# Performance work log

Measured on AMD Instinct MI355X. Metric: run time of the kernel, lower is better.

The kernel has to match this reference:

```python
import jax, jax.numpy as jnp
import numpy as np

H_DIM = 1024
HEAD_SIZE = 1024


def setup_inputs() -> dict:
    key = jax.random.key(0)
    ks = jax.random.split(key, 7)
    s = 1.0 / np.sqrt(H_DIM)
    x = jax.random.normal(ks[0], (4, 4096, H_DIM), dtype=jnp.float32)
    Wq = jax.random.uniform(ks[1], (H_DIM, HEAD_SIZE), jnp.float32, -s, s)
    bq = jax.random.uniform(ks[2], (HEAD_SIZE,), jnp.float32, -s, s)
    Wk = jax.random.uniform(ks[3], (H_DIM, HEAD_SIZE), jnp.float32, -s, s)
    bk = jax.random.uniform(ks[4], (HEAD_SIZE,), jnp.float32, -s, s)
    Wv = jax.random.uniform(ks[5], (H_DIM, HEAD_SIZE), jnp.float32, -s, s)
    bv = jax.random.uniform(ks[6], (HEAD_SIZE,), jnp.float32, -s, s)
    return {"x": x, "Wq": Wq, "bq": bq, "Wk": Wk, "bk": bk, "Wv": Wv, "bv": bv}


def reference(x, Wq, bq, Wk, bk, Wv, bv):
    B, S, _ = x.shape
    q = x @ Wq + bq  # [B,S,hs]
    k = x @ Wk + bk
    v = x @ Wv + bv
    scores = jnp.einsum('bqd,bkd->bqk', q, k)  # [B,S,S]
    causal = jnp.tril(jnp.ones((S, S), dtype=bool))
    scores = jnp.where(causal, scores, -jnp.inf)
    # original divides after masking; -inf stays -inf so math is identical
    w = jax.nn.softmax(scores / jnp.sqrt(jnp.float32(HEAD_SIZE)), axis=-1)
    # dropout p=0.0 -> identity
    return jnp.einsum('bqk,bkd->bqd', w, v)
```

## Files before the change

kernel.cpp:

```cpp
#include <hip/hip_runtime.h>
#include <stdint.h>

typedef _Float16 f16;
typedef _Float16 v8h __attribute__((ext_vector_type(8)));
typedef _Float16 v4h __attribute__((ext_vector_type(4)));
typedef float v4f __attribute__((ext_vector_type(4)));

#define LOG2E 1.44269504088896340736f
#define PT 16384

__device__ __forceinline__ void gll16(const void* g, void* l) {
  __builtin_amdgcn_global_load_lds((__attribute__((address_space(1))) void*)g,
                                   (__attribute__((address_space(3))) void*)l,
                                   16, 0, 0);
}

__device__ __forceinline__ int xcd_swz(int p, int chunk) {
  return (p & 7) * chunk + (p >> 3);
}

__global__ void k_cvt_x(const float* __restrict__ x, f16* __restrict__ xh, int n4) {
  int i = blockIdx.x * blockDim.x + threadIdx.x;
  if (i >= n4) return;
  float4 v = ((const float4*)x)[i];
  v4h o;
  o[0] = (f16)v.x; o[1] = (f16)v.y; o[2] = (f16)v.z; o[3] = (f16)v.w;
  ((v4h*)xh)[i] = o;
}

__global__ void k_cvt_wt(const float* __restrict__ Wq, const float* __restrict__ Wk,
                         const float* __restrict__ Wv, f16* __restrict__ Wt) {
  __shared__ f16 tile[64][65];
  int z = blockIdx.z;
  const float* W = (z == 0) ? Wq : (z == 1) ? Wk : Wv;
  int k0 = blockIdx.y * 64, n0 = blockIdx.x * 64;
  int t = threadIdx.x;
  int r = t >> 4, c4 = t & 15;
  for (int i = 0; i < 4; ++i) {
    int row = r + i * 16;
    float4 v = *(const float4*)&W[(size_t)(k0 + row) * 1024 + n0 + c4 * 4];
    tile[c4 * 4 + 0][row] = (f16)v.x;
    tile[c4 * 4 + 1][row] = (f16)v.y;
    tile[c4 * 4 + 2][row] = (f16)v.z;
    tile[c4 * 4 + 3][row] = (f16)v.w;
  }
  __syncthreads();
  f16* out = Wt + (size_t)z * 1048576;
  for (int i = 0; i < 4; ++i) {
    int n = r + i * 16;
    v4h o;
    o[0] = tile[n][c4 * 4 + 0];
    o[1] = tile[n][c4 * 4 + 1];
    o[2] = tile[n][c4 * 4 + 2];
    o[3] = tile[n][c4 * 4 + 3];
    *(v4h*)&out[(size_t)(n0 + n) * 1024 + k0 + c4 * 4] = o;
  }
}

__global__ __launch_bounds__(512) void k_qkv(
    const f16* __restrict__ xh,
    const f16* __restrict__ Wt,
    const float* __restrict__ bq, const float* __restrict__ bk, const float* __restrict__ bv,
    f16* __restrict__ q, f16* __restrict__ k, f16* __restrict__ vT) {
  __shared__ __align__(16) f16 As[2][16384];
  __shared__ __align__(16) f16 Bs[2][16384];
  int p = blockIdx.x + 64 * (blockIdx.y + 4 * blockIdx.z);
  int l = xcd_swz(p, 96);
  int mt = l / 12;
  int rem = l - mt * 12;
  int z = rem >> 2, nt = rem & 3;
  int m0 = mt * 256, n0 = nt * 256;
  const f16* gA = xh + (size_t)m0 * 1024;
  const f16* gB = Wt + (size_t)z * 1048576 + (size_t)n0 * 1024;
  const float* bias = (z == 0) ? bq : (z == 1) ? bk : bv;
  int tid = threadIdx.x;
  int lane = tid & 63, wave = tid >> 6;
  int quad = lane >> 4, l15 = lane & 15;
  int wm = (wave >> 2) * 128, wn = (wave & 3) * 64;

  int soff[4], slds[4];
#pragma unroll
  for (int h = 0; h < 4; ++h) {
    int s = h * 512 + tid;
    int row = s >> 3;
    int c = (s & 7) ^ (row & 7);
    soff[h] = row * 1024 + c * 8;
    slds[h] = (h * 512 + wave * 64) * 8;
  }
  v4f acc[8][4] = {};
  v8h a[8], bfr[4];

#define QSTAGE(dst, g, kf) do {                                            \
    _Pragma("unroll") for (int h = 0; h < 4; ++h)                          \
      gll16((g) + soff[h] + (kf), &(dst)[slds[h]]);                        \
  } while (0)

#define QREAD(d, ks) do {                                                  \
    int sl = (((ks) * 4 + quad) ^ (l15 & 7)) * 8;                          \
    _Pragma("unroll") for (int i = 0; i < 8; ++i)                          \
      a[i] = *(const v8h*)&As[d][(wm + i * 16 + l15) * 64 + sl];           \
    _Pragma("unroll") for (int j = 0; j < 4; ++j)                          \
      bfr[j] = *(const v8h*)&Bs[d][(wn + j * 16 + l15) * 64 + sl];         \
  } while (0)

#define QMFMA() do {                                                       \
    __builtin_amdgcn_s_setprio(1);                                         \
    _Pragma("unroll") for (int i = 0; i < 8; ++i)                          \
      _Pragma("unroll") for (int j = 0; j < 4; ++j)                        \
        acc[i][j] = __builtin_amdgcn_mfma_f32_16x16x32_f16(a[i], bfr[j], acc[i][j], 0, 0, 0); \
    __builtin_amdgcn_s_setprio(0);                                         \
  } while (0)

  QSTAGE(As[0], gA, 0);
  QSTAGE(Bs[0], gB, 0);

#pragma unroll 1
  for (int it = 0; it < 7; ++it) {
    int k1 = (2 * it + 1) * 64, k2 = (2 * it + 2) * 64;
    QSTAGE(As[1], gA, k1);
    asm volatile("s_waitcnt vmcnt(4)" ::: "memory");
    __builtin_amdgcn_s_barrier();
    QREAD(0, 0); QMFMA();
    QREAD(0, 1);
    QSTAGE(Bs[1], gB, k1);
    QMFMA();
    __builtin_amdgcn_s_barrier();
    QSTAGE(As[0], gA, k2);
    asm volatile("s_waitcnt vmcnt(4)" ::: "memory");
    __builtin_amdgcn_s_barrier();
    QREAD(1, 0); QMFMA();
    QREAD(1, 1);
    QSTAGE(Bs[0], gB, k2);
    QMFMA();
    __builtin_amdgcn_s_barrier();
  }
  {
    int k1 = 15 * 64;
    QSTAGE(As[1], gA, k1);
    asm volatile("s_waitcnt vmcnt(4)" ::: "memory");
    __builtin_amdgcn_s_barrier();
    QREAD(0, 0); QMFMA();
    QREAD(0, 1);
    QSTAGE(Bs[1], gB, k1);
    QMFMA();
    __builtin_amdgcn_s_barrier();
    asm volatile("s_waitcnt vmcnt(0)" ::: "memory");
    __builtin_amdgcn_s_barrier();
    QREAD(1, 0); QMFMA();
    QREAD(1, 1); QMFMA();
  }
#undef QSTAGE
#undef QREAD
#undef QMFMA

  if (z < 2) {
    f16* outp = (z == 0) ? q : k;
    float scale = (z == 0) ? 0.03125f : 1.0f;
#pragma unroll
    for (int j = 0; j < 4; ++j) {
      int n = n0 + wn + j * 16 + l15;
      float bia = bias[n];
#pragma unroll
      for (int i = 0; i < 8; ++i) {
        int mb = m0 + wm + i * 16 + quad * 4;
#pragma unroll
        for (int r = 0; r < 4; ++r)
          outp[(size_t)(mb + r) * 1024 + n] = (f16)((acc[i][j][r] + bia) * scale);
      }
    }
  } else {
#pragma unroll
    for (int j = 0; j < 4; ++j) {
      int n = n0 + wn + j * 16 + l15;
      float bia = bias[n];
#pragma unroll
      for (int i = 0; i < 8; ++i) {
        int m = m0 + wm + i * 16 + quad * 4;
        int bb = m >> 12, s = m & 4095;
        v4h o;
#pragma unroll
        for (int r = 0; r < 4; ++r) o[r] = (f16)(acc[i][j][r] + bia);
        *(v4h*)&vT[((size_t)bb * 1024 + n) * 4096 + s] = o;
      }
    }
  }
}

__global__ void k_zero(float* __restrict__ p) {
  p[blockIdx.x * 256 + threadIdx.x] = 0.f;
}

__global__ __launch_bounds__(256) void k_sgemm(
    const f16* __restrict__ q, const f16* __restrict__ kmat,
    f16* __restrict__ P, float* __restrict__ rowsum, int b0) {
  __shared__ __align__(16) f16 As[2][8192];
  __shared__ __align__(16) f16 Bs[2][8192];
  int p = blockIdx.x + 528 * blockIdx.y;
  int l = xcd_swz(p, 132);
  int i = (l >= 528) ? l - 528 : l;
  int bb = (l >= 528) ? 1 : 0;
  int b = b0 * 2 + bb;
  int mt = (int)((sqrtf(8.f * i + 1.f) - 1.f) * 0.5f);
  while ((mt + 1) * (mt + 2) / 2 <= i) ++mt;
  while (mt * (mt + 1) / 2 > i) --mt;
  int nt = i - mt * (mt + 1) / 2;
  const f16* A = q + ((size_t)b * 4096 + (size_t)mt * 128) * 1024;
  const f16* B = kmat + ((size_t)b * 4096 + (size_t)nt * 128) * 1024;
  f16* Pt = P + (size_t)bb * 528 * PT + (size_t)i * PT;

  int tid = threadIdx.x;
  int lane = tid & 63, wave = tid >> 6;
  int quad = lane >> 4, l15 = lane & 15;
  int wm = (wave & 1) * 64, wn = (wave >> 1) * 64;

  int soff[4], slds[4];
#pragma unroll
  for (int h = 0; h < 4; ++h) {
    int s = h * 256 + tid;
    int row = s >> 3;
    int c = (s & 7) ^ (row & 7);
    soff[h] = row * 1024 + c * 8;
    slds[h] = (h * 256 + wave * 64) * 8;
  }
  v4f acc[4][4] = {};
  v8h a[4], bf[4];

#define SSTAGE(dst, g, kf) do {                                            \
    _Pragma("unroll") for (int h = 0; h < 4; ++h)                          \
      gll16((g) + soff[h] + (kf), &(dst)[slds[h]]);                        \
  } while (0)

#define SREAD(d, ks) do {                                                  \
    int sl = (((ks) * 4 + quad) ^ (l15 & 7)) * 8;                          \
    _Pragma("unroll") for (int ii = 0; ii < 4; ++ii)                       \
      a[ii] = *(const v8h*)&As[d][(wm + ii * 16 + l15) * 64 + sl];         \
    _Pragma("unroll") for (int j = 0; j < 4; ++j)                          \
      bf[j] = *(const v8h*)&Bs[d][(wn + j * 16 + l15) * 64 + sl];          \
  } while (0)

#define SMFMA() do {                                                       \
    __builtin_amdgcn_s_setprio(1);                                         \
    _Pragma("unroll") for (int ii = 0; ii < 4; ++ii)                       \
      _Pragma("unroll") for (int j = 0; j < 4; ++j)                        \
        acc[ii][j] = __builtin_amdgcn_mfma_f32_16x16x32_f16(a[ii], bf[j], acc[ii][j], 0, 0, 0); \
    __builtin_amdgcn_s_setprio(0);                                         \
  } while (0)

  SSTAGE(As[0], A, 0);
  SSTAGE(Bs[0], B, 0);

#pragma unroll 1
  for (int it = 0; it < 7; ++it) {
    int k1 = (2 * it + 1) * 64, k2 = (2 * it + 2) * 64;
    SSTAGE(As[1], A, k1);
    asm volatile("s_waitcnt vmcnt(4)" ::: "memory");
    __builtin_amdgcn_s_barrier();
    SREAD(0, 0); SMFMA();
    SREAD(0, 1);
    SSTAGE(Bs[1], B, k1);
    SMFMA();
    __builtin_amdgcn_s_barrier();
    SSTAGE(As[0], A, k2);
    asm volatile("s_waitcnt vmcnt(4)" ::: "memory");
    __builtin_amdgcn_s_barrier();
    SREAD(1, 0); SMFMA();
    SREAD(1, 1);
    SSTAGE(Bs[0], B, k2);
    SMFMA();
    __builtin_amdgcn_s_barrier();
  }
  {
    int k1 = 15 * 64;
    SSTAGE(As[1], A, k1);
    asm volatile("s_waitcnt vmcnt(4)" ::: "memory");
    __builtin_amdgcn_s_barrier();
    SREAD(0, 0); SMFMA();
    SREAD(0, 1);
    SSTAGE(Bs[1], B, k1);
    SMFMA();
    __builtin_amdgcn_s_barrier();
    asm volatile("s_waitcnt vmcnt(0)" ::: "memory");
    __builtin_amdgcn_s_barrier();
    SREAD(1, 0); SMFMA();
    SREAD(1, 1); SMFMA();
  }
#undef SSTAGE
#undef SREAD
#undef SMFMA

  bool diag = (nt == mt);
  float* rsb = rowsum + (size_t)b * 4096 + mt * 128;
  for (int ii = 0; ii < 4; ++ii) {
    int rl = wm + ii * 16 + quad * 4;
    for (int r = 0; r < 4; ++r) {
      int row_l = rl + r;
      float rs = 0.f;
      for (int j = 0; j < 4; ++j) {
        int col_l = wn + j * 16 + l15;
        float pv = __builtin_amdgcn_exp2f(acc[ii][j][r] * LOG2E);
        if (diag && col_l > row_l) pv = 0.f;
        Pt[(size_t)row_l * 128 + col_l] = (f16)pv;
        rs += pv;
      }
      rs += __shfl_xor(rs, 1, 64);
      rs += __shfl_xor(rs, 2, 64);
      rs += __shfl_xor(rs, 4, 64);
      rs += __shfl_xor(rs, 8, 64);
      if (l15 == 0) atomicAdd(&rsb[row_l], rs);
    }
  }
}

__global__ __launch_bounds__(256) void k_pv(
    const f16* __restrict__ P, const f16* __restrict__ vT,
    const float* __restrict__ rowsum, float* __restrict__ out, int b0) {
  __shared__ __align__(16) f16 As[2][8192];
  __shared__ __align__(16) f16 Bs[2][4096];
  int p = blockIdx.x + 16 * (blockIdx.y + 16 * blockIdx.z);
  int l = xcd_swz(p, 64);
  int dt = l & 15;
  int pr = (l >> 4) & 15;
  int bb = l >> 8;
  int b = b0 * 2 + bb;
  const f16* Pb = P + (size_t)bb * 528 * PT;
  const f16* Vb = vT + (size_t)b * 1024 * 4096;
  int tid = threadIdx.x;
  int lane = tid & 63, wave = tid >> 6;
  int quad = lane >> 4, l15 = lane & 15;
  int wm = (wave & 1) * 64, wn = (wave >> 1) * 32;

  int aoff[4], aslds[4];
#pragma unroll
  for (int h = 0; h < 4; ++h) {
    int s = h * 256 + tid;
    int row = s >> 3;
    int c = (s & 7) ^ (row & 7);
    aoff[h] = row * 128 + c * 8;
    aslds[h] = (h * 256 + wave * 64) * 8;
  }
  int boff[2], bslds[2];
#pragma unroll
  for (int h = 0; h < 2; ++h) {
    int s = h * 256 + tid;
    int row = s >> 3;
    int c = (s & 7) ^ (row & 7);
    boff[h] = (dt * 64 + row) * 4096 + c * 8;
    bslds[h] = (h * 256 + wave * 64) * 8;
  }
  v8h a[4], b_[2];

#define PSTAGE_A(d, Pt_, kc) do {                                          \
    _Pragma("unroll") for (int h = 0; h < 4; ++h)                          \
      gll16((Pt_) + aoff[h] + (kc), &As[d][aslds[h]]);                     \
  } while (0)
#define PSTAGE_B(d, koff) do {                                             \
    _Pragma("unroll") for (int h = 0; h < 2; ++h)                          \
      gll16(Vb + boff[h] + (koff), &Bs[d][bslds[h]]);                      \
  } while (0)
#define PREAD(d, ks) do {                                                  \
    int sl = (((ks) * 4 + quad) ^ (l15 & 7)) * 8;                          \
    _Pragma("unroll") for (int ii = 0; ii < 4; ++ii)                       \
      a[ii] = *(const v8h*)&As[d][(wm + ii * 16 + l15) * 64 + sl];         \
    _Pragma("unroll") for (int j = 0; j < 2; ++j)                          \
      b_[j] = *(const v8h*)&Bs[d][(wn + j * 16 + l15) * 64 + sl];          \
  } while (0)
#define PMFMA(acc_) do {                                                   \
    __builtin_amdgcn_s_setprio(1);                                         \
    _Pragma("unroll") for (int ii = 0; ii < 4; ++ii)                       \
      _Pragma("unroll") for (int j = 0; j < 2; ++j)                        \
        acc_[ii][j] = __builtin_amdgcn_mfma_f32_16x16x32_f16(a[ii], b_[j], acc_[ii][j], 0, 0, 0); \
    __builtin_amdgcn_s_setprio(0);                                         \
  } while (0)

  for (int half = 0; half < 2; ++half) {
    int mt = half ? (31 - pr) : pr;
    size_t ptri = (size_t)mt * (mt + 1) / 2;
    v4f acc[4][2] = {};
    PSTAGE_A(0, Pb + ptri * PT, 0);
    PSTAGE_B(0, 0);
#pragma unroll 1
    for (int i = 0; i < mt; ++i) {
      const f16* Pti = Pb + (ptri + i) * PT;
      const f16* Ptn = Pti + PT;
      PSTAGE_A(1, Pti, 64);
      asm volatile("s_waitcnt vmcnt(4)" ::: "memory");
      __builtin_amdgcn_s_barrier();
      PREAD(0, 0); PMFMA(acc);
      PREAD(0, 1);
      PSTAGE_B(1, i * 128 + 64);
      PMFMA(acc);
      __builtin_amdgcn_s_barrier();
      PSTAGE_A(0, Ptn, 0);
      asm volatile("s_waitcnt vmcnt(4)" ::: "memory");
      __builtin_amdgcn_s_barrier();
      PREAD(1, 0); PMFMA(acc);
      PREAD(1, 1);
      PSTAGE_B(0, (i + 1) * 128);
      PMFMA(acc);
      __builtin_amdgcn_s_barrier();
    }
    {
      const f16* Pti = Pb + (ptri + mt) * PT;
      PSTAGE_A(1, Pti, 64);
      asm volatile("s_waitcnt vmcnt(4)" ::: "memory");
      __builtin_amdgcn_s_barrier();
      PREAD(0, 0); PMFMA(acc);
      PREAD(0, 1);
      PSTAGE_B(1, mt * 128 + 64);
      PMFMA(acc);
      __builtin_amdgcn_s_barrier();
      asm volatile("s_waitcnt vmcnt(0)" ::: "memory");
      __builtin_amdgcn_s_barrier();
      PREAD(1, 0); PMFMA(acc);
      PREAD(1, 1); PMFMA(acc);
      __builtin_amdgcn_s_barrier();
    }
    const float* rsb = rowsum + (size_t)b * 4096 + mt * 128;
    float* ob = out + ((size_t)b * 4096 + (size_t)mt * 128) * 1024 + dt * 64;
    for (int ii = 0; ii < 4; ++ii) {
      int r0 = wm + ii * 16 + quad * 4;
      for (int r = 0; r < 4; ++r) {
        float inv = 1.0f / rsb[r0 + r];
        for (int j = 0; j < 2; ++j) {
          int cc = wn + j * 16 + l15;
          ob[(size_t)(r0 + r) * 1024 + cc] = acc[ii][j][r] * inv;
        }
      }
    }
  }
#undef PSTAGE_A
#undef PSTAGE_B
#undef PREAD
#undef PMFMA
}

extern "C" void kernel_launch(void* const* d_in, const int* in_sizes, int n_in,
                              void* d_out, int out_size, void* d_ws, size_t ws_size,
                              hipStream_t stream) {
  const float* x  = (const float*)d_in[0];
  const float* Wq = (const float*)d_in[1];
  const float* bq = (const float*)d_in[2];
  const float* Wk = (const float*)d_in[3];
  const float* bk = (const float*)d_in[4];
  const float* Wv = (const float*)d_in[5];
  const float* bv = (const float*)d_in[6];
  float* out = (float*)d_out;
  char* ws = (char*)d_ws;
  f16* xh = (f16*)(ws);
  f16* Wt = (f16*)(ws + 33554432);
  f16* q  = (f16*)(ws + 39845888);
  f16* k  = (f16*)(ws + 73400320);
  f16* vT = (f16*)(ws + 106954752);
  f16* P  = (f16*)(ws);
  float* rowsum = (float*)(ws + 34603008);

  k_cvt_x<<<16384, 256, 0, stream>>>(x, xh, 4194304);
  k_cvt_wt<<<dim3(16, 16, 3), 256, 0, stream>>>(Wq, Wk, Wv, Wt);
  k_qkv<<<dim3(64, 4, 3), 512, 0, stream>>>(xh, Wt, bq, bk, bv, q, k, vT);
  k_zero<<<64, 256, 0, stream>>>(rowsum);
  for (int bp = 0; bp < 2; ++bp) {
    k_sgemm<<<dim3(528, 2), 256, 0, stream>>>(q, k, P, rowsum, bp);
    k_pv<<<dim3(16, 16, 2), 256, 0, stream>>>(P, vT, rowsum, out, bp);
  }
}
```

Before: 450.8 us.

## Deepen GEMM pipelines to multi-stage ring buffers with smaller K tiles

Replaces the double-buffered K=64 staging in the QKV and score GEMMs with a 4-deep ring of K=32 tiles, using a new 4-chunk XOR swizzle and one barrier pair per step. The PV kernel moves to a 3-stage ring of its K=64 tiles. The aim is to keep more global-to-LDS loads in flight and hide memory latency better. The cost is more barriers per unit of MFMA work with the smaller K steps, and the changed LDS footprint may affect occupancy.

```diff
diff --git a/kernel.cpp b/kernel.cpp
--- a/kernel.cpp
+++ b/kernel.cpp
@@ -62,8 +62,8 @@
     const f16* __restrict__ Wt,
     const float* __restrict__ bq, const float* __restrict__ bk, const float* __restrict__ bv,
     f16* __restrict__ q, f16* __restrict__ k, f16* __restrict__ vT) {
-  __shared__ __align__(16) f16 As[2][16384];
-  __shared__ __align__(16) f16 Bs[2][16384];
+  __shared__ __align__(16) f16 As[4][8192];
+  __shared__ __align__(16) f16 Bs[4][8192];
   int p = blockIdx.x + 64 * (blockIdx.y + 4 * blockIdx.z);
   int l = xcd_swz(p, 96);
   int mt = l / 12;
@@ -78,29 +78,32 @@
   int quad = lane >> 4, l15 = lane & 15;
   int wm = (wave >> 2) * 128, wn = (wave & 3) * 64;
 
-  int soff[4], slds[4];
-#pragma unroll
-  for (int h = 0; h < 4; ++h) {
+  int soff[2], slds[2];
+#pragma unroll
+  for (int h = 0; h < 2; ++h) {
     int s = h * 512 + tid;
-    int row = s >> 3;
-    int c = (s & 7) ^ (row & 7);
+    int row = s >> 2, pos = s & 3;
+    int c = pos ^ ((row ^ (row >> 2)) & 3);
     soff[h] = row * 1024 + c * 8;
     slds[h] = (h * 512 + wave * 64) * 8;
   }
+  int kb = (l15 ^ (l15 >> 2)) & 3;
   v4f acc[8][4] = {};
   v8h a[8], bfr[4];
 
-#define QSTAGE(dst, g, kf) do {                                            \
-    _Pragma("unroll") for (int h = 0; h < 4; ++h)                          \
-      gll16((g) + soff[h] + (kf), &(dst)[slds[h]]);                        \
-  } while (0)
-
-#define QREAD(d, ks) do {                                                  \
-    int sl = (((ks) * 4 + quad) ^ (l15 & 7)) * 8;                          \
+#define QSTAGE(d, kf) do {                                                 \
+    _Pragma("unroll") for (int h = 0; h < 2; ++h)                          \
+      gll16(gA + soff[h] + (kf), &As[d][slds[h]]);                         \
+    _Pragma("unroll") for (int h = 0; h < 2; ++h)                          \
+      gll16(gB + soff[h] + (kf), &Bs[d][slds[h]]);                         \
+  } while (0)
+
+#define QREAD(d) do {                                                      \
+    int sl = (quad ^ kb) * 8;                                              \
     _Pragma("unroll") for (int i = 0; i < 8; ++i)                          \
-      a[i] = *(const v8h*)&As[d][(wm + i * 16 + l15) * 64 + sl];           \
+      a[i] = *(const v8h*)&As[d][(wm + i * 16 + l15) * 32 + sl];           \
     _Pragma("unroll") for (int j = 0; j < 4; ++j)                          \
-      bfr[j] = *(const v8h*)&Bs[d][(wn + j * 16 + l15) * 64 + sl];         \
+      bfr[j] = *(const v8h*)&Bs[d][(wn + j * 16 + l15) * 32 + sl];         \
   } while (0)
 
 #define QMFMA() do {                                                       \
@@ -111,44 +114,30 @@
     __builtin_amdgcn_s_setprio(0);                                         \
   } while (0)
 
-  QSTAGE(As[0], gA, 0);
-  QSTAGE(Bs[0], gB, 0);
+  QSTAGE(0, 0);
+  QSTAGE(1, 32);
+  QSTAGE(2, 64);
 
 #pragma unroll 1
-  for (int it = 0; it < 7; ++it) {
-    int k1 = (2 * it + 1) * 64, k2 = (2 * it + 2) * 64;
-    QSTAGE(As[1], gA, k1);
-    asm volatile("s_waitcnt vmcnt(4)" ::: "memory");
-    __builtin_amdgcn_s_barrier();
-    QREAD(0, 0); QMFMA();
-    QREAD(0, 1);
-    QSTAGE(Bs[1], gB, k1);
+  for (int t = 0; t < 29; ++t) {
+    QSTAGE((t + 3) & 3, (t + 3) * 32);
+    asm volatile("s_waitcnt vmcnt(12)" ::: "memory");
+    __builtin_amdgcn_s_barrier();
+    QREAD(t & 3);
     QMFMA();
     __builtin_amdgcn_s_barrier();
-    QSTAGE(As[0], gA, k2);
-    asm volatile("s_waitcnt vmcnt(4)" ::: "memory");
-    __builtin_amdgcn_s_barrier();
-    QREAD(1, 0); QMFMA();
-    QREAD(1, 1);
-    QSTAGE(Bs[0], gB, k2);
-    QMFMA();
-    __builtin_amdgcn_s_barrier();
-  }
-  {
-    int k1 = 15 * 64;
-    QSTAGE(As[1], gA, k1);
-    asm volatile("s_waitcnt vmcnt(4)" ::: "memory");
-    __builtin_amdgcn_s_barrier();
-    QREAD(0, 0); QMFMA();
-    QREAD(0, 1);
-    QSTAGE(Bs[1], gB, k1);
-    QMFMA();
-    __builtin_amdgcn_s_barrier();
-    asm volatile("s_waitcnt vmcnt(0)" ::: "memory");
-    __builtin_amdgcn_s_barrier();
-    QREAD(1, 0); QMFMA();
-    QREAD(1, 1); QMFMA();
-  }
+  }
+  asm volatile("s_waitcnt vmcnt(8)" ::: "memory");
+  __builtin_amdgcn_s_barrier();
+  QREAD(1); QMFMA();
+  __builtin_amdgcn_s_barrier();
+  asm volatile("s_waitcnt vmcnt(4)" ::: "memory");
+  __builtin_amdgcn_s_barrier();
+  QREAD(2); QMFMA();
+  __builtin_amdgcn_s_barrier();
+  asm volatile("s_waitcnt vmcnt(0)" ::: "memory");
+  __builtin_amdgcn_s_barrier();
+  QREAD(3); QMFMA();
 #undef QSTAGE
 #undef QREAD
 #undef QMFMA
@@ -193,8 +182,8 @@
 __global__ __launch_bounds__(256) void k_sgemm(
     const f16* __restrict__ q, const f16* __restrict__ kmat,
     f16* __restrict__ P, float* __restrict__ rowsum, int b0) {
-  __shared__ __align__(16) f16 As[2][8192];
-  __shared__ __align__(16) f16 Bs[2][8192];
+  __shared__ __align__(16) f16 As[4][4096];
+  __shared__ __align__(16) f16 Bs[4][4096];
   int p = blockIdx.x + 528 * blockIdx.y;
   int l = xcd_swz(p, 132);
   int i = (l >= 528) ? l - 528 : l;
@@ -213,29 +202,32 @@
   int quad = lane >> 4, l15 = lane & 15;
   int wm = (wave & 1) * 64, wn = (wave >> 1) * 64;
 
-  int soff[4], slds[4];
-#pragma unroll
-  for (int h = 0; h < 4; ++h) {
+  int soff[2], slds[2];
+#pragma unroll
+  for (int h = 0; h < 2; ++h) {
     int s = h * 256 + tid;
-    int row = s >> 3;
-    int c = (s & 7) ^ (row & 7);
+    int row = s >> 2, pos = s & 3;
+    int c = pos ^ ((row ^ (row >> 2)) & 3);
     soff[h] = row * 1024 + c * 8;
     slds[h] = (h * 256 + wave * 64) * 8;
   }
+  int kb = (l15 ^ (l15 >> 2)) & 3;
   v4f acc[4][4] = {};
   v8h a[4], bf[4];
 
-#define SSTAGE(dst, g, kf) do {                                            \
-    _Pragma("unroll") for (int h = 0; h < 4; ++h)                          \
-      gll16((g) + soff[h] + (kf), &(dst)[slds[h]]);                        \
-  } while (0)
-
-#define SREAD(d, ks) do {                                                  \
-    int sl = (((ks) * 4 + quad) ^ (l15 & 7)) * 8;                          \
+#define SSTAGE(d, kf) do {                                                 \
+    _Pragma("unroll") for (int h = 0; h < 2; ++h)                          \
+      gll16(A + soff[h] + (kf), &As[d][slds[h]]);                          \
+    _Pragma("unroll") for (int h = 0; h < 2; ++h)                          \
+      gll16(B + soff[h] + (kf), &Bs[d][slds[h]]);                          \
+  } while (0)
+
+#define SREAD(d) do {                                                      \
+    int sl = (quad ^ kb) * 8;                                              \
     _Pragma("unroll") for (int ii = 0; ii < 4; ++ii)                       \
-      a[ii] = *(const v8h*)&As[d][(wm + ii * 16 + l15) * 64 + sl];         \
+      a[ii] = *(const v8h*)&As[d][(wm + ii * 16 + l15) * 32 + sl];         \
     _Pragma("unroll") for (int j = 0; j < 4; ++j)                          \
-      bf[j] = *(const v8h*)&Bs[d][(wn + j * 16 + l15) * 64 + sl];          \
+      bf[j] = *(const v8h*)&Bs[d][(wn + j * 16 + l15) * 32 + sl];          \
   } while (0)
 
 #define SMFMA() do {                                                       \
@@ -246,44 +238,30 @@
     __builtin_amdgcn_s_setprio(0);                                         \
   } while (0)
 
-  SSTAGE(As[0], A, 0);
-  SSTAGE(Bs[0], B, 0);
+  SSTAGE(0, 0);
+  SSTAGE(1, 32);
+  SSTAGE(2, 64);
 
 #pragma unroll 1
-  for (int it = 0; it < 7; ++it) {
-    int k1 = (2 * it + 1) * 64, k2 = (2 * it + 2) * 64;
-    SSTAGE(As[1], A, k1);
-    asm volatile("s_waitcnt vmcnt(4)" ::: "memory");
-    __builtin_amdgcn_s_barrier();
-    SREAD(0, 0); SMFMA();
-    SREAD(0, 1);
-    SSTAGE(Bs[1], B, k1);
+  for (int t = 0; t < 29; ++t) {
+    SSTAGE((t + 3) & 3, (t + 3) * 32);
+    asm volatile("s_waitcnt vmcnt(12)" ::: "memory");
+    __builtin_amdgcn_s_barrier();
+    SREAD(t & 3);
     SMFMA();
     __builtin_amdgcn_s_barrier();
-    SSTAGE(As[0], A, k2);
-    asm volatile("s_waitcnt vmcnt(4)" ::: "memory");
-    __builtin_amdgcn_s_barrier();
-    SREAD(1, 0); SMFMA();
-    SREAD(1, 1);
-    SSTAGE(Bs[0], B, k2);
-    SMFMA();
-    __builtin_amdgcn_s_barrier();
-  }
-  {
-    int k1 = 15 * 64;
-    SSTAGE(As[1], A, k1);
-    asm volatile("s_waitcnt vmcnt(4)" ::: "memory");
-    __builtin_amdgcn_s_barrier();
-    SREAD(0, 0); SMFMA();
-    SREAD(0, 1);
-    SSTAGE(Bs[1], B, k1);
-    SMFMA();
-    __builtin_amdgcn_s_barrier();
-    asm volatile("s_waitcnt vmcnt(0)" ::: "memory");
-    __builtin_amdgcn_s_barrier();
-    SREAD(1, 0); SMFMA();
-    SREAD(1, 1); SMFMA();
-  }
+  }
+  asm volatile("s_waitcnt vmcnt(8)" ::: "memory");
+  __builtin_amdgcn_s_barrier();
+  SREAD(1); SMFMA();
+  __builtin_amdgcn_s_barrier();
+  asm volatile("s_waitcnt vmcnt(4)" ::: "memory");
+  __builtin_amdgcn_s_barrier();
+  SREAD(2); SMFMA();
+  __builtin_amdgcn_s_barrier();
+  asm volatile("s_waitcnt vmcnt(0)" ::: "memory");
+  __builtin_amdgcn_s_barrier();
+  SREAD(3); SMFMA();
 #undef SSTAGE
 #undef SREAD
 #undef SMFMA
@@ -314,8 +292,8 @@
 __global__ __launch_bounds__(256) void k_pv(
     const f16* __restrict__ P, const f16* __restrict__ vT,
     const float* __restrict__ rowsum, float* __restrict__ out, int b0) {
-  __shared__ __align__(16) f16 As[2][8192];
-  __shared__ __align__(16) f16 Bs[2][4096];
+  __shared__ __align__(16) f16 As[3][8192];
+  __shared__ __align__(16) f16 Bs[3][4096];
   int p = blockIdx.x + 16 * (blockIdx.y + 16 * blockIdx.z);
   int l = xcd_swz(p, 64);
   int dt = l & 15;
@@ -349,13 +327,12 @@
   }
   v8h a[4], b_[2];
 
-#define PSTAGE_A(d, Pt_, kc) do {                                          \
+#define PSTAGE(d, ss) do {                                                 \
+    const f16* Pts_ = Pb + (ptri + ((ss) >> 1)) * PT + ((ss) & 1) * 64;    \
     _Pragma("unroll") for (int h = 0; h < 4; ++h)                          \
-      gll16((Pt_) + aoff[h] + (kc), &As[d][aslds[h]]);                     \
-  } while (0)
-#define PSTAGE_B(d, koff) do {                                             \
+      gll16(Pts_ + aoff[h], &As[d][aslds[h]]);                             \
     _Pragma("unroll") for (int h = 0; h < 2; ++h)                          \
-      gll16(Vb + boff[h] + (koff), &Bs[d][bslds[h]]);                      \
+      gll16(Vb + boff[h] + (ss) * 64, &Bs[d][bslds[h]]);                   \
   } while (0)
 #define PREAD(d, ks) do {                                                  \
     int sl = (((ks) * 4 + quad) ^ (l15 & 7)) * 8;                          \
@@ -364,57 +341,45 @@
     _Pragma("unroll") for (int j = 0; j < 2; ++j)                          \
       b_[j] = *(const v8h*)&Bs[d][(wn + j * 16 + l15) * 64 + sl];          \
   } while (0)
-#define PMFMA(acc_) do {                                                   \
+#define PMFMA() do {                                                       \
     __builtin_amdgcn_s_setprio(1);                                         \
     _Pragma("unroll") for (int ii = 0; ii < 4; ++ii)                       \
       _Pragma("unroll") for (int j = 0; j < 2; ++j)                        \
-        acc_[ii][j] = __builtin_amdgcn_mfma_f32_16x16x32_f16(a[ii], b_[j], acc_[ii][j], 0, 0, 0); \
+        acc[ii][j] = __builtin_amdgcn_mfma_f32_16x16x32_f16(a[ii], b_[j], acc[ii][j], 0, 0, 0); \
     __builtin_amdgcn_s_setprio(0);                                         \
   } while (0)
 
   for (int half = 0; half < 2; ++half) {
     int mt = half ? (31 - pr) : pr;
     size_t ptri = (size_t)mt * (mt + 1) / 2;
+    int S = 2 * (mt + 1);
     v4f acc[4][2] = {};
-    PSTAGE_A(0, Pb + ptri * PT, 0);
-    PSTAGE_B(0, 0);
+    PSTAGE(0, 0);
+    PSTAGE(1, 1);
+    int cur = 0;
 #pragma unroll 1
-    for (int i = 0; i < mt; ++i) {
-      const f16* Pti = Pb + (ptri + i) * PT;
-      const f16* Ptn = Pti + PT;
-      PSTAGE_A(1, Pti, 64);
-      asm volatile("s_waitcnt vmcnt(4)" ::: "memory");
+    for (int s = 0; s + 2 < S; ++s) {
+      int sb = cur + 2; if (sb > 2) sb -= 3;
+      PSTAGE(sb, s + 2);
+      asm volatile("s_waitcnt vmcnt(12)" ::: "memory");
       __builtin_amdgcn_s_barrier();
-      PREAD(0, 0); PMFMA(acc);
-      PREAD(0, 1);
-      PSTAGE_B(1, i * 128 + 64);
-      PMFMA(acc);
+      PREAD(cur, 0); PMFMA();
+      PREAD(cur, 1); PMFMA();
       __builtin_amdgcn_s_barrier();
-      PSTAGE_A(0, Ptn, 0);
-      asm volatile("s_waitcnt vmcnt(4)" ::: "memory");
-      __builtin_amdgcn_s_barrier();
-      PREAD(1, 0); PMFMA(acc);
-      PREAD(1, 1);
-      PSTAGE_B(0, (i + 1) * 128);
-      PMFMA(acc);
-      __builtin_amdgcn_s_barrier();
+      cur = (cur == 2) ? 0 : cur + 1;
     }
-    {
-      const f16* Pti = Pb + (ptri + mt) * PT;
-      PSTAGE_A(1, Pti, 64);
-      asm volatile("s_waitcnt vmcnt(4)" ::: "memory");
-      __builtin_amdgcn_s_barrier();
-      PREAD(0, 0); PMFMA(acc);
-      PREAD(0, 1);
-      PSTAGE_B(1, mt * 128 + 64);
-      PMFMA(acc);
-      __builtin_amdgcn_s_barrier();
-      asm volatile("s_waitcnt vmcnt(0)" ::: "memory");
-      __builtin_amdgcn_s_barrier();
-      PREAD(1, 0); PMFMA(acc);
-      PREAD(1, 1); PMFMA(acc);
-      __builtin_amdgcn_s_barrier();
-    }
+    asm volatile("s_waitcnt vmcnt(6)" ::: "memory");
+    __builtin_amdgcn_s_barrier();
+    PREAD(cur, 0); PMFMA();
+    PREAD(cur, 1); PMFMA();
+    __builtin_amdgcn_s_barrier();
+    cur = (cur == 2) ? 0 : cur + 1;
+    asm volatile("s_waitcnt vmcnt(0)" ::: "memory");
+    __builtin_amdgcn_s_barrier();
+    PREAD(cur, 0); PMFMA();
+    PREAD(cur, 1); PMFMA();
+    __builtin_amdgcn_s_barrier();
+
     const float* rsb = rowsum + (size_t)b * 4096 + mt * 128;
     float* ob = out + ((size_t)b * 4096 + (size_t)mt * 128) * 1024 + dt * 64;
     for (int ii = 0; ii < 4; ++ii) {
@@ -428,8 +393,7 @@
       }
     }
   }
-#undef PSTAGE_A
-#undef PSTAGE_B
+#undef PSTAGE
 #undef PREAD
 #undef PMFMA
 }
```

Result: slower. 549.0 us (+21.8%).

## Widen PV output tile to 128 columns with triple-buffered unified staging

Applied to the files above, without the earlier changes.

The P·V kernel now gives each block a 128x128 output tile instead of 128x64, which halves the number of blocks and halves how often each P tile is reread from global memory. A and B loads are merged into one staging step, and the double buffer becomes a three-deep LDS ring so loads run two stages ahead of compute. The cost is more LDS per block (96KB) and more accumulator registers, which may lower occupancy, and a 256-block grid per launch that may underfill the GPU.

```diff
diff --git a/kernel.cpp b/kernel.cpp
--- a/kernel.cpp
+++ b/kernel.cpp
@@ -314,122 +314,100 @@
 __global__ __launch_bounds__(256) void k_pv(
     const f16* __restrict__ P, const f16* __restrict__ vT,
     const float* __restrict__ rowsum, float* __restrict__ out, int b0) {
-  __shared__ __align__(16) f16 As[2][8192];
-  __shared__ __align__(16) f16 Bs[2][4096];
-  int p = blockIdx.x + 16 * (blockIdx.y + 16 * blockIdx.z);
-  int l = xcd_swz(p, 64);
-  int dt = l & 15;
-  int pr = (l >> 4) & 15;
-  int bb = l >> 8;
+  __shared__ __align__(16) f16 As[3][8192];
+  __shared__ __align__(16) f16 Bs[3][8192];
+  int p = blockIdx.x + 8 * (blockIdx.y + 16 * blockIdx.z);
+  int l = xcd_swz(p, 32);
+  int dt = l & 7;
+  int pr = (l >> 3) & 15;
+  int bb = l >> 7;
   int b = b0 * 2 + bb;
   const f16* Pb = P + (size_t)bb * 528 * PT;
   const f16* Vb = vT + (size_t)b * 1024 * 4096;
   int tid = threadIdx.x;
   int lane = tid & 63, wave = tid >> 6;
   int quad = lane >> 4, l15 = lane & 15;
-  int wm = (wave & 1) * 64, wn = (wave >> 1) * 32;
-
-  int aoff[4], aslds[4];
+  int wm = (wave & 1) * 64, wn = (wave >> 1) * 64;
+
+  int aoff[4], boff[4], slds[4];
 #pragma unroll
   for (int h = 0; h < 4; ++h) {
     int s = h * 256 + tid;
     int row = s >> 3;
     int c = (s & 7) ^ (row & 7);
     aoff[h] = row * 128 + c * 8;
-    aslds[h] = (h * 256 + wave * 64) * 8;
-  }
-  int boff[2], bslds[2];
-#pragma unroll
-  for (int h = 0; h < 2; ++h) {
-    int s = h * 256 + tid;
-    int row = s >> 3;
-    int c = (s & 7) ^ (row & 7);
-    boff[h] = (dt * 64 + row) * 4096 + c * 8;
-    bslds[h] = (h * 256 + wave * 64) * 8;
-  }
-  v8h a[4], b_[2];
-
-#define PSTAGE_A(d, Pt_, kc) do {                                          \
+    boff[h] = (dt * 128 + row) * 4096 + c * 8;
+    slds[h] = (h * 256 + wave * 64) * 8;
+  }
+  v8h a[4], b_[4];
+
+#define PSTAGE(d, ss) do {                                                 \
+    const f16* Pts_ = Pb + (ptri + ((ss) >> 1)) * PT + ((ss) & 1) * 64;    \
     _Pragma("unroll") for (int h = 0; h < 4; ++h)                          \
-      gll16((Pt_) + aoff[h] + (kc), &As[d][aslds[h]]);                     \
-  } while (0)
-#define PSTAGE_B(d, koff) do {                                             \
-    _Pragma("unroll") for (int h = 0; h < 2; ++h)                          \
-      gll16(Vb + boff[h] + (koff), &Bs[d][bslds[h]]);                      \
+      gll16(Pts_ + aoff[h], &As[d][slds[h]]);                              \
+    _Pragma("unroll") for (int h = 0; h < 4; ++h)                          \
+      gll16(Vb + boff[h] + (ss) * 64, &Bs[d][slds[h]]);                    \
   } while (0)
 #define PREAD(d, ks) do {                                                  \
     int sl = (((ks) * 4 + quad) ^ (l15 & 7)) * 8;                          \
     _Pragma("unroll") for (int ii = 0; ii < 4; ++ii)                       \
       a[ii] = *(const v8h*)&As[d][(wm + ii * 16 + l15) * 64 + sl];         \
-    _Pragma("unroll") for (int j = 0; j < 2; ++j)                          \
+    _Pragma("unroll") for (int j = 0; j < 4; ++j)                          \
       b_[j] = *(const v8h*)&Bs[d][(wn + j * 16 + l15) * 64 + sl];          \
   } while (0)
-#define PMFMA(acc_) do {                                                   \
+#define PMFMA() do {                                                       \
     __builtin_amdgcn_s_setprio(1);                                         \
     _Pragma("unroll") for (int ii = 0; ii < 4; ++ii)                       \
-      _Pragma("unroll") for (int j = 0; j < 2; ++j)                        \
-        acc_[ii][j] = __builtin_amdgcn_mfma_f32_16x16x32_f16(a[ii], b_[j], acc_[ii][j], 0, 0, 0); \
+      _Pragma("unroll") for (int j = 0; j < 4; ++j)                        \
+        acc[ii][j] = __builtin_amdgcn_mfma_f32_16x16x32_f16(a[ii], b_[j], acc[ii][j], 0, 0, 0); \
     __builtin_amdgcn_s_setprio(0);                                         \
   } while (0)
 
   for (int half = 0; half < 2; ++half) {
     int mt = half ? (31 - pr) : pr;
     size_t ptri = (size_t)mt * (mt + 1) / 2;
-    v4f acc[4][2] = {};
-    PSTAGE_A(0, Pb + ptri * PT, 0);
-    PSTAGE_B(0, 0);
+    int S = 2 * (mt + 1);
+    v4f acc[4][4] = {};
+    PSTAGE(0, 0);
+    PSTAGE(1, 1);
+    int cur = 0;
 #pragma unroll 1
-    for (int i = 0; i < mt; ++i) {
-      const f16* Pti = Pb + (ptri + i) * PT;
-      const f16* Ptn = Pti + PT;
-      PSTAGE_A(1, Pti, 64);
-      asm volatile("s_waitcnt vmcnt(4)" ::: "memory");
+    for (int s = 0; s + 2 < S; ++s) {
+      int sb = cur + 2; if (sb > 2) sb -= 3;
+      PSTAGE(sb, s + 2);
+      asm volatile("s_waitcnt vmcnt(16)" ::: "memory");
       __builtin_amdgcn_s_barrier();
-      PREAD(0, 0); PMFMA(acc);
-      PREAD(0, 1);
-      PSTAGE_B(1, i * 128 + 64);
-      PMFMA(acc);
+      PREAD(cur, 0); PMFMA();
+      PREAD(cur, 1); PMFMA();
       __builtin_amdgcn_s_barrier();
-      PSTAGE_A(0, Ptn, 0);
-      asm volatile("s_waitcnt vmcnt(4)" ::: "memory");
-      __builtin_amdgcn_s_barrier();
-      PREAD(1, 0); PMFMA(acc);
-      PREAD(1, 1);
-      PSTAGE_B(0, (i + 1) * 128);
-      PMFMA(acc);
-      __builtin_amdgcn_s_barrier();
+      cur = (cur == 2) ? 0 : cur + 1;
     }
-    {
-      const f16* Pti = Pb + (ptri + mt) * PT;
-      PSTAGE_A(1, Pti, 64);
-      asm volatile("s_waitcnt vmcnt(4)" ::: "memory");
-      __builtin_amdgcn_s_barrier();
-      PREAD(0, 0); PMFMA(acc);
-      PREAD(0, 1);
-      PSTAGE_B(1, mt * 128 + 64);
-      PMFMA(acc);
-      __builtin_amdgcn_s_barrier();
-      asm volatile("s_waitcnt vmcnt(0)" ::: "memory");
-      __builtin_amdgcn_s_barrier();
-      PREAD(1, 0); PMFMA(acc);
-      PREAD(1, 1); PMFMA(acc);
-      __builtin_amdgcn_s_barrier();
-    }
+    asm volatile("s_waitcnt vmcnt(8)" ::: "memory");
+    __builtin_amdgcn_s_barrier();
+    PREAD(cur, 0); PMFMA();
+    PREAD(cur, 1); PMFMA();
+    __builtin_amdgcn_s_barrier();
+    cur = (cur == 2) ? 0 : cur + 1;
+    asm volatile("s_waitcnt vmcnt(0)" ::: "memory");
+    __builtin_amdgcn_s_barrier();
+    PREAD(cur, 0); PMFMA();
+    PREAD(cur, 1); PMFMA();
+    __builtin_amdgcn_s_barrier();
+
     const float* rsb = rowsum + (size_t)b * 4096 + mt * 128;
-    float* ob = out + ((size_t)b * 4096 + (size_t)mt * 128) * 1024 + dt * 64;
+    float* ob = out + ((size_t)b * 4096 + (size_t)mt * 128) * 1024 + dt * 128;
     for (int ii = 0; ii < 4; ++ii) {
       int r0 = wm + ii * 16 + quad * 4;
       for (int r = 0; r < 4; ++r) {
         float inv = 1.0f / rsb[r0 + r];
-        for (int j = 0; j < 2; ++j) {
+        for (int j = 0; j < 4; ++j) {
           int cc = wn + j * 16 + l15;
           ob[(size_t)(r0 + r) * 1024 + cc] = acc[ii][j][r] * inv;
         }
       }
     }
   }
-#undef PSTAGE_A
-#undef PSTAGE_B
+#undef PSTAGE
 #undef PREAD
 #undef PMFMA
 }
@@ -460,6 +438,6 @@
   k_zero<<<64, 256, 0, stream>>>(rowsum);
   for (int bp = 0; bp < 2; ++bp) {
     k_sgemm<<<dim3(528, 2), 256, 0, stream>>>(q, k, P, rowsum, bp);
-    k_pv<<<dim3(16, 16, 2), 256, 0, stream>>>(P, vT, rowsum, out, bp);
-  }
-}
+    k_pv<<<dim3(8, 16, 2), 256, 0, stream>>>(P, vT, rowsum, out, bp);
+  }
+}
```

After: 495.4 us. 1.1x slower.
